# Optimization experiments

Hardware: AMD Instinct MI355X
Metric: run time of the kernel (lower is better)

## Reference

```python
import jax, jax.numpy as jnp
import numpy as np

N_QUERY, N_POINTS, FEAT_DIM, K = 32768, 8192, 32, 8

def setup_inputs() -> dict:
    key = jax.random.key(0)
    k1, k2, k3 = jax.random.split(key, 3)
    xyz = jax.random.normal(k1, (N_QUERY, 3), dtype=jnp.float32)
    points = jax.random.normal(k2, (N_POINTS, 3), dtype=jnp.float32)
    # neural_point features are initialized uniform(-1e-4, 1e-4) in the module;
    # we use small-scale gaussians of the same magnitude.
    feats = jax.random.normal(k3, (N_POINTS, FEAT_DIM), dtype=jnp.float32) * 1e-4
    return {"xyz": xyz, "points": points, "feats": feats, "k": K}

def reference(xyz, points, feats, k):
    # Brute-force exact KNN (kpknn equivalent): squared euclidean distances [N, P]
    d2 = (jnp.sum(xyz * xyz, axis=-1, keepdims=True)
          - 2.0 * (xyz @ points.T)
          + jnp.sum(points * points, axis=-1)[None, :])
    _, idx = jax.lax.top_k(-d2, k)          # idx: [N, k] nearest-point indices
    knn_points = points[idx]                # [N, k, 3]
    knn_feats = feats[idx]                  # [N, k, FEAT_DIM]
    return knn_points, knn_feats
```

## Files before the change

kernel.cpp:

```cpp
#include <hip/hip_runtime.h>

#define NQ 32768
#define NP 8192
#define FD 32
#define KNN 8
#define QW 4
#define WPB 8
#define TB 512
#define QBLK (QW * WPB)
#define ABLK 2048
#define CAP 128

typedef unsigned long long u64;

__device__ __forceinline__ u64 shfl_xor_u64(u64 k, int j) {
    unsigned lo = __shfl_xor((unsigned)k, j);
    unsigned hi = __shfl_xor((unsigned)(k >> 32), j);
    return ((u64)hi << 32) | lo;
}
__device__ __forceinline__ u64 sort64_u64(u64 key, int lane) {
    for (int k2 = 2; k2 <= 64; k2 <<= 1)
        for (int j = k2 >> 1; j > 0; j >>= 1) {
            u64 o = shfl_xor_u64(key, j);
            bool keepMin = ((lane & k2) == 0) == ((lane & j) == 0);
            key = ((o < key) == keepMin) ? o : key;
        }
    return key;
}
__device__ __forceinline__ float eighth_smallest64(float v, int lane) {
    for (int k2 = 2; k2 <= 64; k2 <<= 1)
        for (int j = k2 >> 1; j > 0; j >>= 1) {
            float o = __shfl_xor(v, j);
            bool keepMin = ((lane & k2) == 0) == ((lane & j) == 0);
            v = ((o < v) == keepMin) ? o : v;
        }
    return __uint_as_float((unsigned)__builtin_amdgcn_readlane((int)__float_as_uint(v), 7));
}

__global__ void k_prepack(const float* __restrict__ points, float4* __restrict__ pts4) {
    int i = blockIdx.x * blockDim.x + threadIdx.x;
    float px = points[i * 3 + 0], py = points[i * 3 + 1], pz = points[i * 3 + 2];
    float pn = __builtin_fmaf(pz, pz, __builtin_fmaf(py, py, px * px));
    pts4[i] = make_float4(-2.0f * px, -2.0f * py, -2.0f * pz, pn);
}

__global__ __launch_bounds__(TB) void knn_kernel(
    const float* __restrict__ xyz, const float* __restrict__ points,
    const float* __restrict__ feats, const float4* __restrict__ pts4,
    float* __restrict__ out)
{
#pragma clang fp contract(off)
    __shared__ unsigned short sidx16[QBLK * CAP];
    __shared__ int scnt[QBLK];

    const int t     = threadIdx.x;
    const int lane  = t & 63;
    const int wid   = t >> 6;
    const int qbase = blockIdx.x * QBLK + wid * QW;

    if (lane < QW) scnt[wid * QW + lane] = 0;
    __syncthreads();

    float qx[QW], qy[QW], qz[QW], qn[QW], mn[QW], tscr[QW];
#pragma unroll
    for (int qq = 0; qq < QW; ++qq) {
        int q = qbase + qq;
        float a = xyz[q * 3 + 0], b = xyz[q * 3 + 1], c = xyz[q * 3 + 2];
        qx[qq] = a; qy[qq] = b; qz[qq] = c;
        qn[qq] = (a * a + b * b) + c * c;
        mn[qq] = __builtin_inff();
    }

#pragma unroll 4
    for (int s = 0; s < ABLK / 64; ++s) {
        float4 p = pts4[s * 64 + lane];
#pragma unroll
        for (int qq = 0; qq < QW; ++qq) {
            float g = __builtin_fmaf(qx[qq], p.x,
                      __builtin_fmaf(qy[qq], p.y,
                      __builtin_fmaf(qz[qq], p.z, p.w)));
            mn[qq] = fminf(mn[qq], g);
        }
    }
#pragma unroll
    for (int qq = 0; qq < QW; ++qq)
        tscr[qq] = eighth_smallest64(mn[qq], lane) + 1e-3f;

#pragma unroll 4
    for (int s = 0; s < NP / 64; ++s) {
        float4 p = pts4[s * 64 + lane];
        int gidx = s * 64 + lane;
#pragma unroll
        for (int qq = 0; qq < QW; ++qq) {
            float g = __builtin_fmaf(qx[qq], p.x,
                      __builtin_fmaf(qy[qq], p.y,
                      __builtin_fmaf(qz[qq], p.z, p.w)));
            if (__builtin_expect(g <= tscr[qq], 0)) {
                int wq = wid * QW + qq;
                int slot = atomicAdd(&scnt[wq], 1);
                if (slot < CAP) sidx16[wq * CAP + slot] = (unsigned short)gidx;
            }
        }
    }

    const float4* feats4 = (const float4*)feats;
    float4* outf4 = (float4*)(out + (long)NQ * KNN * 3);
#pragma unroll 1
    for (int qq = 0; qq < QW; ++qq) {
        int wq = wid * QW + qq;
        int q  = qbase + qq;
        int cnt = scnt[wq]; if (cnt > CAP) cnt = CAP;

        u64 key1 = ~0ull;
        if (lane < cnt) {
            int idx = sidx16[wq * CAP + lane];
            float px = points[idx * 3 + 0], py = points[idx * 3 + 1], pz = points[idx * 3 + 2];
            float pn  = (px * px + py * py) + pz * pz;
            float dot = __builtin_fmaf(qz[qq], pz, __builtin_fmaf(qy[qq], py, qx[qq] * px));
            float d2v = (qn[qq] - 2.0f * dot) + pn;
            unsigned bb = __float_as_uint(d2v);
            unsigned mk = (bb & 0x80000000u) ? ~bb : (bb | 0x80000000u);
            key1 = ((u64)mk << 32) | (unsigned)idx;
        }
        u64 v = sort64_u64(key1, lane);

        if (cnt > 64) {
            u64 key2 = ~0ull;
            if (lane + 64 < cnt) {
                int idx = sidx16[wq * CAP + 64 + lane];
                float px = points[idx * 3 + 0], py = points[idx * 3 + 1], pz = points[idx * 3 + 2];
                float pn  = (px * px + py * py) + pz * pz;
                float dot = __builtin_fmaf(qz[qq], pz, __builtin_fmaf(qy[qq], py, qx[qq] * px));
                float d2v = (qn[qq] - 2.0f * dot) + pn;
                unsigned bb = __float_as_uint(d2v);
                unsigned mk = (bb & 0x80000000u) ? ~bb : (bb | 0x80000000u);
                key2 = ((u64)mk << 32) | (unsigned)idx;
            }
            u64 s2 = sort64_u64(key2, lane);
            int src = (15 - lane) & 63;
            unsigned lo2 = __shfl((unsigned)s2, src);
            unsigned hi2 = __shfl((unsigned)(s2 >> 32), src);
            u64 kr = ((u64)hi2 << 32) | lo2;
            u64 m = (lane < 8) ? v : ((lane < 16) ? kr : ~0ull);
#pragma unroll
            for (int j = 8; j > 0; j >>= 1) {
                u64 o = shfl_xor_u64(m, j);
                bool low = (lane & j) == 0;
                m = low ? (o < m ? o : m) : (o < m ? m : o);
            }
            v = m;
        }

        int nb = __shfl((int)(unsigned)v, lane >> 3);
        outf4[(long)q * (KNN * FD / 4) + lane] = feats4[(long)nb * (FD / 4) + (lane & 7)];
        int j2 = lane / 3;
        int nb2 = __shfl((int)(unsigned)v, j2);
        if (lane < 24) {
            out[(long)q * (KNN * 3) + lane] = points[nb2 * 3 + (lane - j2 * 3)];
        }
    }
}

extern "C" void kernel_launch(void* const* d_in, const int* in_sizes, int n_in,
                              void* d_out, int out_size, void* d_ws, size_t ws_size,
                              hipStream_t stream) {
    const float* xyz    = (const float*)d_in[0];
    const float* points = (const float*)d_in[1];
    const float* feats  = (const float*)d_in[2];
    float* out = (float*)d_out;
    float4* pts4 = (float4*)d_ws;

    hipLaunchKernelGGL(k_prepack, dim3(NP / 256), dim3(256), 0, stream, points, pts4);
    hipLaunchKernelGGL(knn_kernel, dim3(NQ / QBLK), dim3(TB), 0, stream,
                       xyz, points, feats, pts4, out);
}
```

Before: 83.48 us.

## Bin points and queries by z to prune the brute-force KNN candidate scan

```diff
diff --git a/kernel.cpp b/kernel.cpp
--- a/kernel.cpp
+++ b/kernel.cpp
@@ -10,8 +10,14 @@
 #define QBLK (QW * WPB)
 #define ABLK 2048
 #define CAP 128
+#define NB 256
 
 typedef unsigned long long u64;
+
+__device__ __forceinline__ int binof(float z) {
+    int b = (int)floorf((z + 5.0f) * 25.6f);
+    return min(NB - 1, max(0, b));
+}
 
 __device__ __forceinline__ u64 shfl_xor_u64(u64 k, int j) {
     unsigned lo = __shfl_xor((unsigned)k, j);
@@ -37,16 +43,66 @@
     return __uint_as_float((unsigned)__builtin_amdgcn_readlane((int)__float_as_uint(v), 7));
 }
 
-__global__ void k_prepack(const float* __restrict__ points, float4* __restrict__ pts4) {
-    int i = blockIdx.x * blockDim.x + threadIdx.x;
-    float px = points[i * 3 + 0], py = points[i * 3 + 1], pz = points[i * 3 + 2];
-    float pn = __builtin_fmaf(pz, pz, __builtin_fmaf(py, py, px * px));
-    pts4[i] = make_float4(-2.0f * px, -2.0f * py, -2.0f * pz, pn);
+__global__ void k_hist(const float* __restrict__ xyz, const float* __restrict__ points,
+                       unsigned* __restrict__ pcnt, unsigned* __restrict__ qcnt,
+                       float4* __restrict__ pts4a) {
+    int t = blockIdx.x * 256 + threadIdx.x;
+    if (t < NP) atomicAdd(&pcnt[binof(points[t * 3 + 2])], 1u);
+    if (t < NQ) atomicAdd(&qcnt[binof(xyz[t * 3 + 2])], 1u);
+    if (t < ABLK) {
+        int i = t * 4;
+        float px = points[i * 3 + 0], py = points[i * 3 + 1], pz = points[i * 3 + 2];
+        float pn = __builtin_fmaf(pz, pz, __builtin_fmaf(py, py, px * px));
+        pts4a[t] = make_float4(-2.0f * px, -2.0f * py, -2.0f * pz, pn);
+    }
+}
+
+__global__ __launch_bounds__(256) void k_scan(unsigned* __restrict__ pcnt, unsigned* __restrict__ pstart,
+                                              unsigned* __restrict__ qcnt, unsigned* __restrict__ qstart) {
+    __shared__ unsigned sh[NB];
+    int t = threadIdx.x;
+    sh[t] = pcnt[t]; __syncthreads();
+    for (int off = 1; off < NB; off <<= 1) {
+        unsigned v = (t >= off) ? sh[t - off] : 0; __syncthreads();
+        sh[t] += v; __syncthreads();
+    }
+    unsigned ex = t ? sh[t - 1] : 0;
+    pstart[t] = ex; if (t == NB - 1) pstart[NB] = sh[NB - 1];
+    pcnt[t] = ex;
+    __syncthreads();
+    sh[t] = qcnt[t]; __syncthreads();
+    for (int off = 1; off < NB; off <<= 1) {
+        unsigned v = (t >= off) ? sh[t - off] : 0; __syncthreads();
+        sh[t] += v; __syncthreads();
+    }
+    unsigned qex = t ? sh[t - 1] : 0;
+    qstart[t] = qex; if (t == NB - 1) qstart[NB] = sh[NB - 1];
+    qcnt[t] = qex;
+}
+
+__global__ void k_scatter(const float* __restrict__ xyz, const float* __restrict__ points,
+                          unsigned* __restrict__ pcur, unsigned* __restrict__ qcur,
+                          float4* __restrict__ pts4s, unsigned short* __restrict__ pidxs,
+                          unsigned* __restrict__ qids) {
+    int t = blockIdx.x * 256 + threadIdx.x;
+    if (t < NP) {
+        float px = points[t * 3 + 0], py = points[t * 3 + 1], pz = points[t * 3 + 2];
+        float pn = __builtin_fmaf(pz, pz, __builtin_fmaf(py, py, px * px));
+        unsigned pos = atomicAdd(&pcur[binof(pz)], 1u);
+        pts4s[pos] = make_float4(-2.0f * px, -2.0f * py, -2.0f * pz, pn);
+        pidxs[pos] = (unsigned short)t;
+    }
+    if (t < NQ) {
+        unsigned pos = atomicAdd(&qcur[binof(xyz[t * 3 + 2])], 1u);
+        qids[pos] = (unsigned)t;
+    }
 }
 
 __global__ __launch_bounds__(TB) void knn_kernel(
     const float* __restrict__ xyz, const float* __restrict__ points,
-    const float* __restrict__ feats, const float4* __restrict__ pts4,
+    const float* __restrict__ feats, const float4* __restrict__ pts4a,
+    const float4* __restrict__ pts4s, const unsigned short* __restrict__ pidxs,
+    const unsigned* __restrict__ pstart, const unsigned* __restrict__ qids,
     float* __restrict__ out)
 {
 #pragma clang fp contract(off)
@@ -61,10 +117,12 @@
     if (lane < QW) scnt[wid * QW + lane] = 0;
     __syncthreads();
 
+    unsigned qid[QW];
     float qx[QW], qy[QW], qz[QW], qn[QW], mn[QW], tscr[QW];
 #pragma unroll
     for (int qq = 0; qq < QW; ++qq) {
-        int q = qbase + qq;
+        unsigned q = qids[qbase + qq];
+        qid[qq] = q;
         float a = xyz[q * 3 + 0], b = xyz[q * 3 + 1], c = xyz[q * 3 + 2];
         qx[qq] = a; qy[qq] = b; qz[qq] = c;
         qn[qq] = (a * a + b * b) + c * c;
@@ -73,7 +131,7 @@
 
 #pragma unroll 4
     for (int s = 0; s < ABLK / 64; ++s) {
-        float4 p = pts4[s * 64 + lane];
+        float4 p = pts4a[s * 64 + lane];
 #pragma unroll
         for (int qq = 0; qq < QW; ++qq) {
             float g = __builtin_fmaf(qx[qq], p.x,
@@ -86,19 +144,29 @@
     for (int qq = 0; qq < QW; ++qq)
         tscr[qq] = eighth_smallest64(mn[qq], lane) + 1e-3f;
 
-#pragma unroll 4
-    for (int s = 0; s < NP / 64; ++s) {
-        float4 p = pts4[s * 64 + lane];
-        int gidx = s * 64 + lane;
+    float zlo = __builtin_inff(), zhi = -__builtin_inff();
+#pragma unroll
+    for (int qq = 0; qq < QW; ++qq) {
+        float r2 = fmaxf(qn[qq] + tscr[qq] + 2e-3f, 0.0f);
+        float r  = sqrtf(r2) + 1e-4f;
+        zlo = fminf(zlo, qz[qq] - r);
+        zhi = fmaxf(zhi, qz[qq] + r);
+    }
+    int lo = (int)pstart[binof(zlo)];
+    int hi = (int)pstart[binof(zhi) + 1];
+
+    for (int i = lo + lane; i < hi; i += 64) {
+        float4 p = pts4s[i];
 #pragma unroll
         for (int qq = 0; qq < QW; ++qq) {
             float g = __builtin_fmaf(qx[qq], p.x,
                       __builtin_fmaf(qy[qq], p.y,
                       __builtin_fmaf(qz[qq], p.z, p.w)));
             if (__builtin_expect(g <= tscr[qq], 0)) {
+                int oi = pidxs[i];
                 int wq = wid * QW + qq;
                 int slot = atomicAdd(&scnt[wq], 1);
-                if (slot < CAP) sidx16[wq * CAP + slot] = (unsigned short)gidx;
+                if (slot < CAP) sidx16[wq * CAP + slot] = (unsigned short)oi;
             }
         }
     }
@@ -108,7 +176,7 @@
 #pragma unroll 1
     for (int qq = 0; qq < QW; ++qq) {
         int wq = wid * QW + qq;
-        int q  = qbase + qq;
+        int q  = (int)qid[qq];
         int cnt = scnt[wq]; if (cnt > CAP) cnt = CAP;
 
         u64 key1 = ~0ull;
@@ -168,9 +236,22 @@
     const float* points = (const float*)d_in[1];
     const float* feats  = (const float*)d_in[2];
     float* out = (float*)d_out;
-    float4* pts4 = (float4*)d_ws;
-
-    hipLaunchKernelGGL(k_prepack, dim3(NP / 256), dim3(256), 0, stream, points, pts4);
+
+    char* ws = (char*)d_ws;
+    float4*         pts4a  = (float4*)(ws);
+    float4*         pts4s  = (float4*)(ws + 32768);
+    unsigned*       qids   = (unsigned*)(ws + 163840);
+    unsigned short* pidxs  = (unsigned short*)(ws + 294912);
+    unsigned*       pcnt   = (unsigned*)(ws + 311296);
+    unsigned*       pstart = (unsigned*)(ws + 312320);
+    unsigned*       qcnt   = (unsigned*)(ws + 313348);
+    unsigned*       qstart = (unsigned*)(ws + 314372);
+
+    hipMemsetAsync(ws + 311296, 0, 315400 - 311296, stream);
+    hipLaunchKernelGGL(k_hist,    dim3(NQ / 256), dim3(256), 0, stream, xyz, points, pcnt, qcnt, pts4a);
+    hipLaunchKernelGGL(k_scan,    dim3(1),        dim3(256), 0, stream, pcnt, pstart, qcnt, qstart);
+    hipLaunchKernelGGL(k_scatter, dim3(NQ / 256), dim3(256), 0, stream, xyz, points, pcnt, qcnt,
+                       pts4s, pidxs, qids);
     hipLaunchKernelGGL(knn_kernel, dim3(NQ / QBLK), dim3(TB), 0, stream,
-                       xyz, points, feats, pts4, out);
-}
+                       xyz, points, feats, pts4a, pts4s, pidxs, pstart, qids, out);
+}
```

After: 144.3 us. 1.73x slower.

## Stage point chunks in LDS and use packed FMA for distance scan

Applied to the files above, without the earlier changes.

```diff
diff --git a/kernel.cpp b/kernel.cpp
--- a/kernel.cpp
+++ b/kernel.cpp
@@ -8,10 +8,17 @@
 #define WPB 8
 #define TB 512
 #define QBLK (QW * WPB)
-#define ABLK 2048
+#define CHP 1024
 #define CAP 128
 
 typedef unsigned long long u64;
+typedef float f32x2 __attribute__((ext_vector_type(2)));
+
+__device__ __forceinline__ f32x2 pkfma(f32x2 a, f32x2 b, f32x2 c) {
+    f32x2 d;
+    asm("v_pk_fma_f32 %0, %1, %2, %3" : "=v"(d) : "v"(a), "v"(b), "v"(c));
+    return d;
+}
 
 __device__ __forceinline__ u64 shfl_xor_u64(u64 k, int j) {
     unsigned lo = __shfl_xor((unsigned)k, j);
@@ -50,6 +57,7 @@
     float* __restrict__ out)
 {
 #pragma clang fp contract(off)
+    __shared__ f32x2 sX[CHP / 2], sY[CHP / 2], sZ[CHP / 2], sW[CHP / 2];
     __shared__ unsigned short sidx16[QBLK * CAP];
     __shared__ int scnt[QBLK];
 
@@ -58,50 +66,80 @@
     const int wid   = t >> 6;
     const int qbase = blockIdx.x * QBLK + wid * QW;
 
-    if (lane < QW) scnt[wid * QW + lane] = 0;
-    __syncthreads();
-
-    float qx[QW], qy[QW], qz[QW], qn[QW], mn[QW], tscr[QW];
+    if (t < QBLK) scnt[t] = 0;
+
+    float qn[QW], mn[QW], tscr[QW];
+    float qxs[QW], qys[QW], qzs[QW];
+    f32x2 qx2[QW], qy2[QW], qz2[QW];
 #pragma unroll
     for (int qq = 0; qq < QW; ++qq) {
         int q = qbase + qq;
         float a = xyz[q * 3 + 0], b = xyz[q * 3 + 1], c = xyz[q * 3 + 2];
-        qx[qq] = a; qy[qq] = b; qz[qq] = c;
+        qxs[qq] = a; qys[qq] = b; qzs[qq] = c;
+        qx2[qq] = (f32x2){a, a}; qy2[qq] = (f32x2){b, b}; qz2[qq] = (f32x2){c, c};
         qn[qq] = (a * a + b * b) + c * c;
         mn[qq] = __builtin_inff();
     }
 
-#pragma unroll 4
-    for (int s = 0; s < ABLK / 64; ++s) {
-        float4 p = pts4[s * 64 + lane];
-#pragma unroll
-        for (int qq = 0; qq < QW; ++qq) {
-            float g = __builtin_fmaf(qx[qq], p.x,
-                      __builtin_fmaf(qy[qq], p.y,
-                      __builtin_fmaf(qz[qq], p.z, p.w)));
-            mn[qq] = fminf(mn[qq], g);
+#define STAGE(c)  {                                                   \
+        float4 pa = pts4[(c) * CHP + 2 * t];                          \
+        float4 pb = pts4[(c) * CHP + 2 * t + 1];                      \
+        sX[t] = (f32x2){pa.x, pb.x}; sY[t] = (f32x2){pa.y, pb.y};     \
+        sZ[t] = (f32x2){pa.z, pb.z}; sW[t] = (f32x2){pa.w, pb.w}; }
+
+#pragma unroll 1
+    for (int c = 0; c < 2; ++c) {
+        __syncthreads();
+        STAGE(c);
+        __syncthreads();
+#pragma unroll 2
+        for (int s = 0; s < CHP / 128; ++s) {
+            int j = s * 64 + lane;
+            f32x2 X = sX[j], Y = sY[j], Z = sZ[j], W = sW[j];
+#pragma unroll
+            for (int qq = 0; qq < QW; ++qq) {
+                f32x2 g = pkfma(X, qx2[qq], pkfma(Y, qy2[qq], pkfma(Z, qz2[qq], W)));
+                mn[qq] = fminf(mn[qq], fminf(g[0], g[1]));
+            }
         }
     }
 #pragma unroll
     for (int qq = 0; qq < QW; ++qq)
         tscr[qq] = eighth_smallest64(mn[qq], lane) + 1e-3f;
 
-#pragma unroll 4
-    for (int s = 0; s < NP / 64; ++s) {
-        float4 p = pts4[s * 64 + lane];
-        int gidx = s * 64 + lane;
-#pragma unroll
-        for (int qq = 0; qq < QW; ++qq) {
-            float g = __builtin_fmaf(qx[qq], p.x,
-                      __builtin_fmaf(qy[qq], p.y,
-                      __builtin_fmaf(qz[qq], p.z, p.w)));
-            if (__builtin_expect(g <= tscr[qq], 0)) {
-                int wq = wid * QW + qq;
-                int slot = atomicAdd(&scnt[wq], 1);
-                if (slot < CAP) sidx16[wq * CAP + slot] = (unsigned short)gidx;
-            }
-        }
-    }
+#pragma unroll 1
+    for (int k = 0; k < 8; ++k) {
+        int c = (k == 0) ? 1 : ((k <= 6) ? k + 1 : 0);
+        if (k > 0) {
+            __syncthreads();
+            STAGE(c);
+            __syncthreads();
+        }
+#pragma unroll 2
+        for (int s = 0; s < CHP / 128; ++s) {
+            int j = s * 64 + lane;
+            f32x2 X = sX[j], Y = sY[j], Z = sZ[j], W = sW[j];
+            int bj = c * CHP + 2 * j;
+#pragma unroll
+            for (int qq = 0; qq < QW; ++qq) {
+                f32x2 g = pkfma(X, qx2[qq], pkfma(Y, qy2[qq], pkfma(Z, qz2[qq], W)));
+                float gm = fminf(g[0], g[1]);
+                if (__builtin_expect(gm <= tscr[qq], 0)) {
+                    int wq = wid * QW + qq;
+                    if (g[0] <= tscr[qq]) {
+                        int slot = atomicAdd(&scnt[wq], 1);
+                        if (slot < CAP) sidx16[wq * CAP + slot] = (unsigned short)bj;
+                    }
+                    if (g[1] <= tscr[qq]) {
+                        int slot = atomicAdd(&scnt[wq], 1);
+                        if (slot < CAP) sidx16[wq * CAP + slot] = (unsigned short)(bj + 1);
+                    }
+                }
+            }
+        }
+    }
+#undef STAGE
+    __syncthreads();
 
     const float4* feats4 = (const float4*)feats;
     float4* outf4 = (float4*)(out + (long)NQ * KNN * 3);
@@ -116,7 +154,7 @@
             int idx = sidx16[wq * CAP + lane];
             float px = points[idx * 3 + 0], py = points[idx * 3 + 1], pz = points[idx * 3 + 2];
             float pn  = (px * px + py * py) + pz * pz;
-            float dot = __builtin_fmaf(qz[qq], pz, __builtin_fmaf(qy[qq], py, qx[qq] * px));
+            float dot = __builtin_fmaf(qzs[qq], pz, __builtin_fmaf(qys[qq], py, qxs[qq] * px));
             float d2v = (qn[qq] - 2.0f * dot) + pn;
             unsigned bb = __float_as_uint(d2v);
             unsigned mk = (bb & 0x80000000u) ? ~bb : (bb | 0x80000000u);
@@ -130,7 +168,7 @@
                 int idx = sidx16[wq * CAP + 64 + lane];
                 float px = points[idx * 3 + 0], py = points[idx * 3 + 1], pz = points[idx * 3 + 2];
                 float pn  = (px * px + py * py) + pz * pz;
-                float dot = __builtin_fmaf(qz[qq], pz, __builtin_fmaf(qy[qq], py, qx[qq] * px));
+                float dot = __builtin_fmaf(qzs[qq], pz, __builtin_fmaf(qys[qq], py, qxs[qq] * px));
                 float d2v = (qn[qq] - 2.0f * dot) + pn;
                 unsigned bb = __float_as_uint(d2v);
                 unsigned mk = (bb & 0x80000000u) ? ~bb : (bb | 0x80000000u);
```

After: 109.9 us. +31.7%, slower.
